# Optimization experiments

Measured on AMD Instinct MI355X. Metric: run time of the kernel, lower is better.

The kernel has to match this reference:

```python
import jax, jax.numpy as jnp
import numpy as np

N_NODES = 50000
N_EDGES = 800000
IN_DIM, HID, OUT_DIM = 32, 96, 1
NEG_SLOPE = 0.2


def _glorot(key, shape):
    fan_in, fan_out = shape[0], shape[-1]
    lim = float(np.sqrt(6.0 / (fan_in + fan_out)))
    return jax.random.uniform(key, shape, jnp.float32, -lim, lim)


def setup_inputs() -> dict:
    key = jax.random.key(0)
    ks = jax.random.split(key, 20)
    inp = {
        "x": jax.random.normal(ks[0], (N_NODES, IN_DIM), jnp.float32),
        "edge_index": jax.random.randint(ks[1], (2, N_EDGES), 0, N_NODES, jnp.int64),
        "edge_weight": jax.random.uniform(ks[2], (N_EDGES,), jnp.float32),
    }
    dims = [(IN_DIM, HID), (HID, HID), (HID, HID), (HID, OUT_DIM)]
    names = ["0", "1", "2", "f"]
    k = 3
    for nm, (di, do) in zip(names, dims):
        inp["W" + nm] = _glorot(ks[k], (di, do)); k += 1
        inp["as" + nm] = _glorot(ks[k], (1, do))[0]; k += 1
        inp["ad" + nm] = _glorot(ks[k], (1, do))[0]; k += 1
        inp["b" + nm] = jnp.zeros((do,), jnp.float32)
    return inp


def _gat_conv(x, src, dst, n, W, a_s, a_d, b):
    # h: [N, out]; per-node attention logits, gathered per edge
    h = x @ W
    es = h @ a_s  # [N]
    ed = h @ a_d  # [N]
    e = jax.nn.leaky_relu(es[src] + ed[dst], NEG_SLOPE)  # [E]
    m = jax.ops.segment_max(e, dst, num_segments=n)  # segment-softmax (stable)
    ex = jnp.exp(e - m[dst])
    s = jax.ops.segment_sum(ex, dst, num_segments=n)
    alpha = ex / s[dst]  # every node has a self loop -> s > 0
    out = jax.ops.segment_sum(alpha[:, None] * h[src], dst, num_segments=n)
    return out + b


def reference(x, edge_index, edge_weight, W0, as0, ad0, b0, W1, as1, ad1, b1,
              W2, as2, ad2, b2, Wf, asf, adf, bf):
    # edge_weight is ignored: PyG GATConv with edge_dim=None drops edge_attr.
    n = x.shape[0]
    loops = jnp.arange(n, dtype=edge_index.dtype)
    src = jnp.concatenate([edge_index[0], loops])  # add_self_loops=True
    dst = jnp.concatenate([edge_index[1], loops])

    # dropout is identity in eval mode
    for (W, a_s, a_d, b) in [(W0, as0, ad0, b0), (W1, as1, ad1, b1), (W2, as2, ad2, b2)]:
        residual = x
        x = _gat_conv(x, src, dst, n, W, a_s, a_d, b)
        if x.shape == residual.shape:
            x = x + residual
        x = jax.nn.relu(x)
    return _gat_conv(x, src, dst, n, Wf, asf, adf, bf)
```

## Files before the change

kernel.cpp:

```cpp
#include <hip/hip_runtime.h>
#include <hip/hip_fp16.h>
#include <math.h>

#define N_NODES 50000
#define N_EDGES 800000
#define E_TOT   (N_EDGES + N_NODES)
#define IN_DIM  32
#define HID     96
#define NEG_SLOPE 0.2f
#define BUCKET  48
#define G_PAD   50
#define NBINS   196
#define BCAP    5120
#define GC_STRIDE 64
#define FILL_EPT 16
#define FILL_NB ((N_EDGES + 256 * FILL_EPT - 1) / (256 * FILL_EPT))
#define AGG_BLOCKS (N_NODES / 16)
#define PREP_BLOCKS ((N_NODES * 32) / 256)
#define WT_BLOCKS (((HID * HID) + 255) / 256)

typedef _Float16 half8v __attribute__((ext_vector_type(8)));
typedef float    float4v __attribute__((ext_vector_type(4)));

static inline int cdiv(long long a, int b) { return (int)((a + b - 1) / b); }

__device__ __forceinline__ int clamp_src(int s) {
    return (int)min((unsigned)s, (unsigned)(N_NODES - 1));
}

__global__ __launch_bounds__(256) void build_prep_kernel(
    const int* __restrict__ ei, unsigned* __restrict__ gcnt,
    unsigned* __restrict__ ebuf,
    const float* __restrict__ x, const float* __restrict__ W0,
    const float* __restrict__ as0, const float* __restrict__ ad0,
    __half* __restrict__ xh, float* __restrict__ es, float* __restrict__ ed,
    const float* __restrict__ W1, const float* __restrict__ W2,
    __half* __restrict__ WT1, __half* __restrict__ WT2) {
    int b = blockIdx.x;
    if (b < FILL_NB) {
        __shared__ unsigned lcnt[256];
        __shared__ unsigned lbase[256];
        int tid = threadIdx.x;
        lcnt[tid] = 0u;
        __syncthreads();
        int e0 = (b * 256 + tid) * FILL_EPT;
        bool val = e0 < N_EDGES;
        unsigned pk[FILL_EPT];
        unsigned short rank[FILL_EPT];
        if (val) {
            #pragma unroll
            for (int q = 0; q < FILL_EPT / 4; ++q) {
                int4 d4 = *(const int4*)(ei + N_EDGES + e0 + q * 4);
                int4 s4 = *(const int4*)(ei + e0 + q * 4);
                int dd[4] = {d4.x, d4.y, d4.z, d4.w};
                int ss[4] = {s4.x, s4.y, s4.z, s4.w};
                #pragma unroll
                for (int k = 0; k < 4; ++k) {
                    int d = clamp_src(dd[k]);
                    int bin = d >> 8;
                    pk[q * 4 + k] = (unsigned)clamp_src(ss[k]) | ((unsigned)(d & 255) << 16)
                                  | ((unsigned)bin << 24);
                    rank[q * 4 + k] = (unsigned short)atomicAdd(&lcnt[bin], 1u);
                }
            }
        }
        __syncthreads();
        if (tid < NBINS) {
            unsigned c = lcnt[tid];
            lbase[tid] = c ? atomicAdd(gcnt + (size_t)tid * GC_STRIDE, c) : 0u;
        }
        __syncthreads();
        if (val) {
            #pragma unroll
            for (int k = 0; k < FILL_EPT; ++k) {
                unsigned bin = pk[k] >> 24;
                unsigned pos = lbase[bin] + rank[k];
                if (pos < BCAP) ebuf[(size_t)bin * BCAP + pos] = pk[k];
            }
        }
        return;
    }
    b -= FILL_NB;
    if (b >= PREP_BLOCKS) {
        int i = (b - PREP_BLOCKS) * 256 + threadIdx.x;
        if (i < HID * HID) {
            int n = i / HID, k = i - n * HID;
            WT1[i] = __float2half(W1[k * HID + n]);
            WT2[i] = __float2half(W2[k * HID + n]);
        }
        return;
    }
    __shared__ float s_us[32], s_ud[32];
    if (threadIdx.x < 64) {
        int k = threadIdx.x & 31;
        int sel = threadIdx.x >> 5;
        const float* a = sel ? ad0 : as0;
        float acc = 0.f;
        #pragma unroll 8
        for (int c = 0; c < HID; ++c) acc += W0[k * HID + c] * a[c];
        if (sel) s_ud[k] = acc; else s_us[k] = acc;
    }
    __syncthreads();
    int idx = b * 256 + threadIdx.x;
    int node = idx >> 5;
    int k = threadIdx.x & 31;
    float xv = x[(size_t)node * 32 + k];
    float xnb = __shfl_xor(xv, 1);
    if ((k & 1) == 0) {
        __half2 h2v = __floats2half2_rn(xv, xnb);
        ((__half2*)xh)[((size_t)node * 32 + k) >> 1] = h2v;
    }
    float ps = xv * s_us[k], pd = xv * s_ud[k];
    #pragma unroll
    for (int o = 16; o; o >>= 1) {
        ps += __shfl_xor(ps, o);
        pd += __shfl_xor(pd, o);
    }
    if (k == 0) { es[node] = ps; ed[node] = pd; }
}

__global__ __launch_bounds__(256) void bucket_build_kernel(
    const unsigned* __restrict__ gcnt, const unsigned* __restrict__ ebuf,
    unsigned* __restrict__ cnt, unsigned short* __restrict__ srcs) {
    __shared__ unsigned short lsr[256][BUCKET];
    __shared__ unsigned lct[256];
    int bin = blockIdx.x, tid = threadIdx.x;
    int nb = bin * 256 + tid;
    lct[tid] = 1u;
    lsr[tid][0] = (unsigned short)min(nb, N_NODES - 1);
    __syncthreads();
    unsigned ec = min(gcnt[(size_t)bin * GC_STRIDE], (unsigned)BCAP);
    for (unsigned j = tid; j < ec; j += 256) {
        unsigned pkv = ebuf[(size_t)bin * BCAP + j];
        unsigned dloc = (pkv >> 16) & 255u;
        unsigned pos = atomicAdd(&lct[dloc], 1u);
        if (pos < BUCKET) lsr[dloc][pos] = (unsigned short)(pkv & 0xFFFFu);
    }
    __syncthreads();
    if (nb < N_NODES) cnt[nb] = min(lct[tid], (unsigned)BUCKET);
    const uint4* ls4 = (const uint4*)&lsr[0][0];
    uint4* gs4 = (uint4*)(srcs + (size_t)bin * 256 * BUCKET);
    for (int i = tid; i < 256 * (BUCKET / 8); i += 256) {
        int node = i / (BUCKET / 8);
        if (bin * 256 + node < N_NODES) gs4[i] = ls4[i];
    }
}

__global__ __launch_bounds__(256) void aggregate32_kernel(
    const unsigned* __restrict__ cnt, const unsigned short* __restrict__ srcs,
    const float* __restrict__ es, const float* __restrict__ ed,
    const __half* __restrict__ xh,
    const float* __restrict__ W0, const float* __restrict__ b0,
    __half* __restrict__ x16a) {
    __shared__ uint2 sh[4][4][G_PAD];
    __shared__ float s_ag[16][33];
    __shared__ float4 s_w0[32][24];
    const float4* W4g = (const float4*)W0;
    for (int i = threadIdx.x; i < 32 * 24; i += 256)
        s_w0[i / 24][i % 24] = W4g[i];

    int lane = threadIdx.x & 63;
    int wv = threadIdx.x >> 6;
    int g = lane >> 4, lin = lane & 15;
    int node = blockIdx.x * 16 + wv * 4 + g;
    size_t row = (size_t)node * BUCKET;
    int deg = min((int)cnt[node], BUCKET);
    float edv = ed[node];

    float lsum = 0.f;
    float4 acc = {0.f, 0.f, 0.f, 0.f};
    const uint2* x2 = (const uint2*)xh;
    int h8sel = lin >> 3;
    int c = lin & 7;

    for (int j = lin; j < deg; j += 16) {
        int s = clamp_src(srcs[row + j]);
        float v = es[s] + edv;
        v = v > 0.f ? v : NEG_SLOPE * v;
        float e = __expf(v);
        uint2 p; p.x = (unsigned)s; p.y = __float_as_uint(e);
        sh[wv][g][j] = p;
        lsum += e;
    }
    int j = 0;
    for (; j + 8 <= deg; j += 8) {
        uint2 p0 = sh[wv][g][j + h8sel];
        uint2 p1 = sh[wv][g][j + 2 + h8sel];
        uint2 p2 = sh[wv][g][j + 4 + h8sel];
        uint2 p3 = sh[wv][g][j + 6 + h8sel];
        uint2 q0 = x2[(size_t)p0.x * 8 + c];
        uint2 q1 = x2[(size_t)p1.x * 8 + c];
        uint2 q2 = x2[(size_t)p2.x * 8 + c];
        uint2 q3 = x2[(size_t)p3.x * 8 + c];
        float e0 = __uint_as_float(p0.y), e1 = __uint_as_float(p1.y);
        float e2 = __uint_as_float(p2.y), e3 = __uint_as_float(p3.y);
        float2 f00 = __half22float2(*(__half2*)&q0.x), f01 = __half22float2(*(__half2*)&q0.y);
        float2 f10 = __half22float2(*(__half2*)&q1.x), f11 = __half22float2(*(__half2*)&q1.y);
        float2 f20 = __half22float2(*(__half2*)&q2.x), f21 = __half22float2(*(__half2*)&q2.y);
        float2 f30 = __half22float2(*(__half2*)&q3.x), f31 = __half22float2(*(__half2*)&q3.y);
        acc.x += e0 * f00.x + e1 * f10.x + e2 * f20.x + e3 * f30.x;
        acc.y += e0 * f00.y + e1 * f10.y + e2 * f20.y + e3 * f30.y;
        acc.z += e0 * f01.x + e1 * f11.x + e2 * f21.x + e3 * f31.x;
        acc.w += e0 * f01.y + e1 * f11.y + e2 * f21.y + e3 * f31.y;
    }
    for (; j + 4 <= deg; j += 4) {
        uint2 p0 = sh[wv][g][j + h8sel];
        uint2 p1 = sh[wv][g][j + 2 + h8sel];
        uint2 q0 = x2[(size_t)p0.x * 8 + c];
        uint2 q1 = x2[(size_t)p1.x * 8 + c];
        float e0 = __uint_as_float(p0.y), e1 = __uint_as_float(p1.y);
        float2 f00 = __half22float2(*(__half2*)&q0.x), f01 = __half22float2(*(__half2*)&q0.y);
        float2 f10 = __half22float2(*(__half2*)&q1.x), f11 = __half22float2(*(__half2*)&q1.y);
        acc.x += e0 * f00.x + e1 * f10.x; acc.y += e0 * f00.y + e1 * f10.y;
        acc.z += e0 * f01.x + e1 * f11.x; acc.w += e0 * f01.y + e1 * f11.y;
    }
    for (; j < deg; j += 2) {
        int idx = j + h8sel;
        if (idx < deg) {
            uint2 p = sh[wv][g][idx];
            uint2 q = x2[(size_t)p.x * 8 + c];
            float e = __uint_as_float(p.y);
            float2 f0 = __half22float2(*(__half2*)&q.x);
            float2 f1 = __half22float2(*(__half2*)&q.y);
            acc.x += e * f0.x; acc.y += e * f0.y;
            acc.z += e * f1.x; acc.w += e * f1.y;
        }
    }
    #pragma unroll
    for (int o = 1; o < 16; o <<= 1) lsum += __shfl_xor(lsum, o);
    acc.x += __shfl_xor(acc.x, 8);
    acc.y += __shfl_xor(acc.y, 8);
    acc.z += __shfl_xor(acc.z, 8);
    acc.w += __shfl_xor(acc.w, 8);
    if (lin < 8) {
        float inv = 1.f / lsum;
        int n = wv * 4 + g;
        s_ag[n][lin * 4 + 0] = acc.x * inv;
        s_ag[n][lin * 4 + 1] = acc.y * inv;
        s_ag[n][lin * 4 + 2] = acc.z * inv;
        s_ag[n][lin * 4 + 3] = acc.w * inv;
    }
    __syncthreads();
    int t = threadIdx.x;
    if (t < 192) {
        int n = t / 12, c8 = t - n * 12;
        int onode = blockIdx.x * 16 + n;
        float4 a0v = {0.f, 0.f, 0.f, 0.f}, a1v = {0.f, 0.f, 0.f, 0.f};
        #pragma unroll 8
        for (int k = 0; k < 32; ++k) {
            float a = s_ag[n][k];
            float4 w0 = s_w0[k][c8 * 2], w1 = s_w0[k][c8 * 2 + 1];
            a0v.x += a * w0.x; a0v.y += a * w0.y; a0v.z += a * w0.z; a0v.w += a * w0.w;
            a1v.x += a * w1.x; a1v.y += a * w1.y; a1v.z += a * w1.z; a1v.w += a * w1.w;
        }
        float4 bb0 = ((const float4*)b0)[c8 * 2], bb1 = ((const float4*)b0)[c8 * 2 + 1];
        float v0 = fmaxf(a0v.x + bb0.x, 0.f), v1 = fmaxf(a0v.y + bb0.y, 0.f);
        float v2 = fmaxf(a0v.z + bb0.z, 0.f), v3 = fmaxf(a0v.w + bb0.w, 0.f);
        float v4 = fmaxf(a1v.x + bb1.x, 0.f), v5 = fmaxf(a1v.y + bb1.y, 0.f);
        float v6 = fmaxf(a1v.z + bb1.z, 0.f), v7 = fmaxf(a1v.w + bb1.w, 0.f);
        __half2 q0 = __floats2half2_rn(v0, v1), q1 = __floats2half2_rn(v2, v3);
        __half2 q2 = __floats2half2_rn(v4, v5), q3 = __floats2half2_rn(v6, v7);
        uint4 st; st.x = *(unsigned*)&q0; st.y = *(unsigned*)&q1;
        st.z = *(unsigned*)&q2; st.w = *(unsigned*)&q3;
        ((uint4*)x16a)[(size_t)onode * 12 + c8] = st;
    }
}

__global__ __launch_bounds__(256) void mfma_gemm96_kernel(
    const __half* __restrict__ x16, const __half* __restrict__ wt,
    const float* __restrict__ a_s, const float* __restrict__ a_d,
    __half* __restrict__ h, float* __restrict__ es, float* __restrict__ ed) {
    __shared__ __align__(16) __half s_t[4][16][104];
    int wid = (int)((blockIdx.x * 256 + threadIdx.x) >> 6);
    if (wid >= N_NODES / 16) return;
    int lane = threadIdx.x & 63;
    int wvl = threadIdx.x >> 6;
    int col = lane & 15, quad = lane >> 4;
    int m0 = wid * 16;
    const __half* arow = x16 + (size_t)(m0 + col) * 96 + quad * 8;
    const __half* brow = wt + (size_t)col * 96 + quad * 8;

    float4v acc[6];
    #pragma unroll
    for (int t = 0; t < 6; ++t) acc[t] = (float4v){0.f, 0.f, 0.f, 0.f};

    #pragma unroll
    for (int ks = 0; ks < 3; ++ks) {
        half8v afrag = *(const half8v*)(arow + ks * 32);
        #pragma unroll
        for (int t = 0; t < 6; ++t) {
            half8v bfrag = *(const half8v*)(brow + (size_t)t * 16 * 96 + ks * 32);
            acc[t] = __builtin_amdgcn_mfma_f32_16x16x32_f16(afrag, bfrag, acc[t], 0, 0, 0);
        }
    }

    float ps0 = 0.f, ps1 = 0.f, ps2 = 0.f, ps3 = 0.f;
    float pd0 = 0.f, pd1 = 0.f, pd2 = 0.f, pd3 = 0.f;
    #pragma unroll
    for (int t = 0; t < 6; ++t) {
        int ch = t * 16 + col;
        float sa = a_s[ch], sd = a_d[ch];
        float v0 = acc[t][0], v1 = acc[t][1], v2 = acc[t][2], v3 = acc[t][3];
        int r0 = quad * 4;
        s_t[wvl][r0 + 0][ch] = __float2half(v0);
        s_t[wvl][r0 + 1][ch] = __float2half(v1);
        s_t[wvl][r0 + 2][ch] = __float2half(v2);
        s_t[wvl][r0 + 3][ch] = __float2half(v3);
        ps0 += v0 * sa; ps1 += v1 * sa; ps2 += v2 * sa; ps3 += v3 * sa;
        pd0 += v0 * sd; pd1 += v1 * sd; pd2 += v2 * sd; pd3 += v3 * sd;
    }
    #pragma unroll
    for (int o = 1; o < 16; o <<= 1) {
        ps0 += __shfl_xor(ps0, o); ps1 += __shfl_xor(ps1, o);
        ps2 += __shfl_xor(ps2, o); ps3 += __shfl_xor(ps3, o);
        pd0 += __shfl_xor(pd0, o); pd1 += __shfl_xor(pd1, o);
        pd2 += __shfl_xor(pd2, o); pd3 += __shfl_xor(pd3, o);
    }
    if (col == 0) {
        int nb = m0 + quad * 4;
        es[nb] = ps0; es[nb + 1] = ps1; es[nb + 2] = ps2; es[nb + 3] = ps3;
        ed[nb] = pd0; ed[nb + 1] = pd1; ed[nb + 2] = pd2; ed[nb + 3] = pd3;
    }
    {
        int trow = lane >> 2, q = lane & 3;
        const uint4* sr = (const uint4*)&s_t[wvl][trow][0];
        uint4* H8 = (uint4*)h;
        size_t rb = (size_t)(m0 + trow) * 12;
        H8[rb + q]     = sr[q];
        H8[rb + q + 4] = sr[q + 4];
        H8[rb + q + 8] = sr[q + 8];
    }
}

__global__ __launch_bounds__(256) void aggregate96_kernel(
    const unsigned* __restrict__ cnt, const unsigned short* __restrict__ srcs,
    const float* __restrict__ es, const float* __restrict__ ed,
    const __half* __restrict__ h, const float* __restrict__ b,
    const __half* __restrict__ res16, __half* __restrict__ out16,
    const float* __restrict__ Wf, float* __restrict__ hfin, int do_relu) {
    __shared__ uint2 sh[4][4][G_PAD];
    int lane = threadIdx.x & 63;
    int wv = threadIdx.x >> 6;
    int g = lane >> 4, lin = lane & 15;
    int node = blockIdx.x * 16 + wv * 4 + g;
    size_t row = (size_t)node * BUCKET;
    int deg = min((int)cnt[node], BUCKET);
    float edv = ed[node];

    float lsum = 0.f;
    float a0 = 0.f, a1 = 0.f, a2 = 0.f, a3 = 0.f, a4 = 0.f, a5 = 0.f, a6 = 0.f, a7 = 0.f;
    const uint4* h8 = (const uint4*)h;
    bool act = (lin < 12);

    for (int j = lin; j < deg; j += 16) {
        int s = clamp_src(srcs[row + j]);
        float v = es[s] + edv;
        v = v > 0.f ? v : NEG_SLOPE * v;
        float e = __expf(v);
        uint2 p; p.x = (unsigned)s; p.y = __float_as_uint(e);
        sh[wv][g][j] = p;
        lsum += e;
    }
    int j = 0;
    for (; j + 4 <= deg; j += 4) {
        uint2 p0 = sh[wv][g][j];
        uint2 p1 = sh[wv][g][j + 1];
        uint2 p2 = sh[wv][g][j + 2];
        uint2 p3 = sh[wv][g][j + 3];
        if (act) {
            uint4 q0 = h8[(size_t)p0.x * 12 + lin];
            uint4 q1 = h8[(size_t)p1.x * 12 + lin];
            uint4 q2 = h8[(size_t)p2.x * 12 + lin];
            uint4 q3 = h8[(size_t)p3.x * 12 + lin];
            float e0 = __uint_as_float(p0.y), e1 = __uint_as_float(p1.y);
            float e2 = __uint_as_float(p2.y), e3 = __uint_as_float(p3.y);
            float2 fa0 = __half22float2(*(__half2*)&q0.x), fa1 = __half22float2(*(__half2*)&q0.y);
            float2 fa2 = __half22float2(*(__half2*)&q0.z), fa3 = __half22float2(*(__half2*)&q0.w);
            float2 fb0 = __half22float2(*(__half2*)&q1.x), fb1 = __half22float2(*(__half2*)&q1.y);
            float2 fb2 = __half22float2(*(__half2*)&q1.z), fb3 = __half22float2(*(__half2*)&q1.w);
            float2 fc0 = __half22float2(*(__half2*)&q2.x), fc1 = __half22float2(*(__half2*)&q2.y);
            float2 fc2 = __half22float2(*(__half2*)&q2.z), fc3 = __half22float2(*(__half2*)&q2.w);
            float2 fd0 = __half22float2(*(__half2*)&q3.x), fd1 = __half22float2(*(__half2*)&q3.y);
            float2 fd2 = __half22float2(*(__half2*)&q3.z), fd3 = __half22float2(*(__half2*)&q3.w);
            a0 += e0 * fa0.x + e1 * fb0.x + e2 * fc0.x + e3 * fd0.x;
            a1 += e0 * fa0.y + e1 * fb0.y + e2 * fc0.y + e3 * fd0.y;
            a2 += e0 * fa1.x + e1 * fb1.x + e2 * fc1.x + e3 * fd1.x;
            a3 += e0 * fa1.y + e1 * fb1.y + e2 * fc1.y + e3 * fd1.y;
            a4 += e0 * fa2.x + e1 * fb2.x + e2 * fc2.x + e3 * fd2.x;
            a5 += e0 * fa2.y + e1 * fb2.y + e2 * fc2.y + e3 * fd2.y;
            a6 += e0 * fa3.x + e1 * fb3.x + e2 * fc3.x + e3 * fd3.x;
            a7 += e0 * fa3.y + e1 * fb3.y + e2 * fc3.y + e3 * fd3.y;
        }
    }
    for (; j < deg; ++j) {
        uint2 p = sh[wv][g][j];
        if (act) {
            uint4 q = h8[(size_t)p.x * 12 + lin];
            float e = __uint_as_float(p.y);
            float2 f0 = __half22float2(*(__half2*)&q.x);
            float2 f1 = __half22float2(*(__half2*)&q.y);
            float2 f2 = __half22float2(*(__half2*)&q.z);
            float2 f3 = __half22float2(*(__half2*)&q.w);
            a0 += e * f0.x; a1 += e * f0.y;
            a2 += e * f1.x; a3 += e * f1.y;
            a4 += e * f2.x; a5 += e * f2.y;
            a6 += e * f3.x; a7 += e * f3.y;
        }
    }
    #pragma unroll
    for (int o = 1; o < 16; o <<= 1) lsum += __shfl_xor(lsum, o);

    float pfin = 0.f;
    if (act) {
        float inv = 1.f / lsum;
        const float4* b4 = (const float4*)b;
        float4 bb0 = b4[lin * 2], bb1 = b4[lin * 2 + 1];
        float v0 = a0 * inv + bb0.x, v1 = a1 * inv + bb0.y;
        float v2 = a2 * inv + bb0.z, v3 = a3 * inv + bb0.w;
        float v4 = a4 * inv + bb1.x, v5 = a5 * inv + bb1.y;
        float v6 = a6 * inv + bb1.z, v7 = a7 * inv + bb1.w;
        if (res16) {
            uint4 rr = ((const uint4*)res16)[(size_t)node * 12 + lin];
            float2 r0 = __half22float2(*(__half2*)&rr.x);
            float2 r1 = __half22float2(*(__half2*)&rr.y);
            float2 r2 = __half22float2(*(__half2*)&rr.z);
            float2 r3 = __half22float2(*(__half2*)&rr.w);
            v0 += r0.x; v1 += r0.y; v2 += r1.x; v3 += r1.y;
            v4 += r2.x; v5 += r2.y; v6 += r3.x; v7 += r3.y;
        }
        if (do_relu) {
            v0 = fmaxf(v0, 0.f); v1 = fmaxf(v1, 0.f); v2 = fmaxf(v2, 0.f); v3 = fmaxf(v3, 0.f);
            v4 = fmaxf(v4, 0.f); v5 = fmaxf(v5, 0.f); v6 = fmaxf(v6, 0.f); v7 = fmaxf(v7, 0.f);
        }
        if (out16) {
            __half2 q0 = __floats2half2_rn(v0, v1), q1 = __floats2half2_rn(v2, v3);
            __half2 q2 = __floats2half2_rn(v4, v5), q3 = __floats2half2_rn(v6, v7);
            uint4 st; st.x = *(unsigned*)&q0; st.y = *(unsigned*)&q1;
            st.z = *(unsigned*)&q2; st.w = *(unsigned*)&q3;
            ((uint4*)out16)[(size_t)node * 12 + lin] = st;
        }
        if (hfin) {
            const float4* w4 = (const float4*)Wf;
            float4 wf0 = w4[lin * 2], wf1 = w4[lin * 2 + 1];
            pfin = v0 * wf0.x + v1 * wf0.y + v2 * wf0.z + v3 * wf0.w
                 + v4 * wf1.x + v5 * wf1.y + v6 * wf1.z + v7 * wf1.w;
        }
    }
    if (hfin) {
        #pragma unroll
        for (int o = 1; o < 16; o <<= 1) pfin += __shfl_xor(pfin, o);
        if (lin == 0) hfin[node] = pfin;
    }
}

__global__ __launch_bounds__(256) void aggregate1_kernel(
    const unsigned* __restrict__ cnt, const unsigned short* __restrict__ srcs,
    const float* __restrict__ hfin, const float* __restrict__ asf,
    const float* __restrict__ adf, const float* __restrict__ bf,
    float* __restrict__ out) {
    int lane = threadIdx.x & 63;
    int wv = threadIdx.x >> 6;
    int g = lane >> 4, lin = lane & 15;
    int node = blockIdx.x * 16 + wv * 4 + g;
    size_t row = (size_t)node * BUCKET;
    int deg = min((int)cnt[node], BUCKET);
    float as0 = asf[0], ad0 = adf[0];
    float edv = hfin[node] * ad0;

    float lsum = 0.f, acc = 0.f;
    for (int j = lin; j < deg; j += 16) {
        int s = clamp_src(srcs[row + j]);
        float hs = hfin[s];
        float v = as0 * hs + edv;
        v = v > 0.f ? v : NEG_SLOPE * v;
        float ex = __expf(v);
        lsum += ex;
        acc += ex * hs;
    }
    #pragma unroll
    for (int o = 1; o < 16; o <<= 1) {
        lsum += __shfl_xor(lsum, o);
        acc  += __shfl_xor(acc, o);
    }
    if (lin == 0) out[node] = acc / lsum + bf[0];
}


extern "C" void kernel_launch(void* const* d_in, const int* in_sizes, int n_in,
                              void* d_out, int out_size, void* d_ws, size_t ws_size,
                              hipStream_t stream) {
    const float* x  = (const float*)d_in[0];
    const int*   ei = (const int*)d_in[1];
    const float* W0 = (const float*)d_in[3];
    const float* as0 = (const float*)d_in[4];
    const float* ad0 = (const float*)d_in[5];
    const float* b0 = (const float*)d_in[6];
    const float* W1 = (const float*)d_in[7];
    const float* as1 = (const float*)d_in[8];
    const float* ad1 = (const float*)d_in[9];
    const float* b1 = (const float*)d_in[10];
    const float* W2 = (const float*)d_in[11];
    const float* as2 = (const float*)d_in[12];
    const float* ad2 = (const float*)d_in[13];
    const float* b2 = (const float*)d_in[14];
    const float* Wf = (const float*)d_in[15];
    const float* asf = (const float*)d_in[16];
    const float* adf = (const float*)d_in[17];
    const float* bf = (const float*)d_in[18];

    float* out = (float*)d_out;

    float* Hf = (float*)d_ws;
    __half* H16 = (__half*)Hf;
    float* ES = Hf + (long long)N_NODES * HID;
    float* ED = ES + N_NODES;
    unsigned* CNT = (unsigned*)(ED + N_NODES);
    unsigned short* SRCS = (unsigned short*)(CNT + N_NODES);
    __half* X16A = (__half*)(SRCS + (size_t)N_NODES * BUCKET);
    __half* X16B = X16A + (size_t)N_NODES * HID;
    __half* WT1 = X16B + (size_t)N_NODES * HID;
    __half* WT2 = WT1 + HID * HID;
    float* HFIN = (float*)(WT2 + HID * HID);
    __half* XH = (__half*)(HFIN + N_NODES);
    unsigned* GCNT = (unsigned*)(XH + (size_t)N_NODES * 32);
    unsigned* EBUF = GCNT + (size_t)NBINS * GC_STRIDE;

    hipMemsetAsync(GCNT, 0, (size_t)NBINS * GC_STRIDE * sizeof(unsigned), stream);
    build_prep_kernel<<<FILL_NB + PREP_BLOCKS + WT_BLOCKS, 256, 0, stream>>>(
        ei, GCNT, EBUF, x, W0, as0, ad0, XH, ES, ED, W1, W2, WT1, WT2);
    bucket_build_kernel<<<NBINS, 256, 0, stream>>>(GCNT, EBUF, CNT, SRCS);

    const int mfma_blocks = cdiv(N_NODES / 16, 4);

    aggregate32_kernel<<<AGG_BLOCKS, 256, 0, stream>>>(CNT, SRCS, ES, ED, XH, W0, b0, X16A);

    mfma_gemm96_kernel<<<mfma_blocks, 256, 0, stream>>>(X16A, WT1, as1, ad1, H16, ES, ED);
    aggregate96_kernel<<<AGG_BLOCKS, 256, 0, stream>>>(
        CNT, SRCS, ES, ED, H16, b1, X16A, X16B, nullptr, nullptr, 1);

    mfma_gemm96_kernel<<<mfma_blocks, 256, 0, stream>>>(X16B, WT2, as2, ad2, H16, ES, ED);
    aggregate96_kernel<<<AGG_BLOCKS, 256, 0, stream>>>(
        CNT, SRCS, ES, ED, H16, b2, X16B, nullptr, Wf, HFIN, 1);

    aggregate1_kernel<<<AGG_BLOCKS, 256, 0, stream>>>(CNT, SRCS, HFIN, asf, adf, bf, out);
}
```

Before: 239.2 us.

## Fuse 96-wide MFMA projection into preceding aggregation kernels

Removes the standalone mfma_gemm96 kernel launches by having each aggregation block stage its 16 output rows in shared memory and run the next layer's MFMA projection plus attention-logit reduction in one wave. Double-buffers H and ES/ED so a kernel can write the next layer's projections while others still read the current ones. This saves two launches and a global reread of the hidden features, at the cost of extra shared memory and a serialized single-wave epilogue per block that leaves three waves idle.

```diff
diff --git a/kernel.cpp b/kernel.cpp
--- a/kernel.cpp
+++ b/kernel.cpp
@@ -26,6 +26,65 @@
 
 __device__ __forceinline__ int clamp_src(int s) {
     return (int)min((unsigned)s, (unsigned)(N_NODES - 1));
+}
+
+__device__ __forceinline__ void mfma_tile_epilogue(
+    const __half* s_x , __half* s_t ,
+    const __half* __restrict__ wt, const float* __restrict__ a_s,
+    const float* __restrict__ a_d, __half* __restrict__ h,
+    float* __restrict__ es, float* __restrict__ ed, int m0, int lane) {
+    int col = lane & 15, quad = lane >> 4;
+    const __half* arow = s_x + col * 104 + quad * 8;
+    const __half* brow = wt + (size_t)col * 96 + quad * 8;
+
+    float4v acc[6];
+    #pragma unroll
+    for (int t = 0; t < 6; ++t) acc[t] = (float4v){0.f, 0.f, 0.f, 0.f};
+    #pragma unroll
+    for (int ks = 0; ks < 3; ++ks) {
+        half8v afrag = *(const half8v*)(arow + ks * 32);
+        #pragma unroll
+        for (int t = 0; t < 6; ++t) {
+            half8v bfrag = *(const half8v*)(brow + (size_t)t * 16 * 96 + ks * 32);
+            acc[t] = __builtin_amdgcn_mfma_f32_16x16x32_f16(afrag, bfrag, acc[t], 0, 0, 0);
+        }
+    }
+    float ps0 = 0.f, ps1 = 0.f, ps2 = 0.f, ps3 = 0.f;
+    float pd0 = 0.f, pd1 = 0.f, pd2 = 0.f, pd3 = 0.f;
+    #pragma unroll
+    for (int t = 0; t < 6; ++t) {
+        int ch = t * 16 + col;
+        float sa = a_s[ch], sd = a_d[ch];
+        float v0 = acc[t][0], v1 = acc[t][1], v2 = acc[t][2], v3 = acc[t][3];
+        int r0 = quad * 4;
+        s_t[(r0 + 0) * 104 + ch] = __float2half(v0);
+        s_t[(r0 + 1) * 104 + ch] = __float2half(v1);
+        s_t[(r0 + 2) * 104 + ch] = __float2half(v2);
+        s_t[(r0 + 3) * 104 + ch] = __float2half(v3);
+        ps0 += v0 * sa; ps1 += v1 * sa; ps2 += v2 * sa; ps3 += v3 * sa;
+        pd0 += v0 * sd; pd1 += v1 * sd; pd2 += v2 * sd; pd3 += v3 * sd;
+    }
+    #pragma unroll
+    for (int o = 1; o < 16; o <<= 1) {
+        ps0 += __shfl_xor(ps0, o); ps1 += __shfl_xor(ps1, o);
+        ps2 += __shfl_xor(ps2, o); ps3 += __shfl_xor(ps3, o);
+        pd0 += __shfl_xor(pd0, o); pd1 += __shfl_xor(pd1, o);
+        pd2 += __shfl_xor(pd2, o); pd3 += __shfl_xor(pd3, o);
+    }
+    if (col == 0) {
+        int nb = m0 + quad * 4;
+        es[nb] = ps0; es[nb + 1] = ps1; es[nb + 2] = ps2; es[nb + 3] = ps3;
+        ed[nb] = pd0; ed[nb + 1] = pd1; ed[nb + 2] = pd2; ed[nb + 3] = pd3;
+    }
+    {
+        int trow = lane >> 2, q = lane & 3;
+        const uint4* sr = (const uint4*)(s_t + trow * 104);
+        uint4* H8 = (uint4*)h;
+        size_t rb = (size_t)(m0 + trow) * 12;
+        H8[rb + q]     = sr[q];
+        H8[rb + q + 4] = sr[q + 4];
+        H8[rb + q + 8] = sr[q + 8];
+    }
 }
 
 __global__ __launch_bounds__(256) void build_prep_kernel(
@@ -151,10 +210,15 @@
     const float* __restrict__ es, const float* __restrict__ ed,
     const __half* __restrict__ xh,
     const float* __restrict__ W0, const float* __restrict__ b0,
-    __half* __restrict__ x16a) {
+    __half* __restrict__ x16a,
+    const __half* __restrict__ wt1, const float* __restrict__ as1,
+    const float* __restrict__ ad1, __half* __restrict__ hA,
+    float* __restrict__ es2, float* __restrict__ ed2) {
     __shared__ uint2 sh[4][4][G_PAD];
     __shared__ float s_ag[16][33];
     __shared__ float4 s_w0[32][24];
+    __shared__ __align__(16) __half s_x[16 * 104];
+    __shared__ __align__(16) __half s_t[16 * 104];
     const float4* W4g = (const float4*)W0;
     for (int i = threadIdx.x; i < 32 * 24; i += 256)
         s_w0[i / 24][i % 24] = W4g[i];
@@ -263,73 +327,12 @@
         uint4 st; st.x = *(unsigned*)&q0; st.y = *(unsigned*)&q1;
         st.z = *(unsigned*)&q2; st.w = *(unsigned*)&q3;
         ((uint4*)x16a)[(size_t)onode * 12 + c8] = st;
-    }
-}
-
-__global__ __launch_bounds__(256) void mfma_gemm96_kernel(
-    const __half* __restrict__ x16, const __half* __restrict__ wt,
-    const float* __restrict__ a_s, const float* __restrict__ a_d,
-    __half* __restrict__ h, float* __restrict__ es, float* __restrict__ ed) {
-    __shared__ __align__(16) __half s_t[4][16][104];
-    int wid = (int)((blockIdx.x * 256 + threadIdx.x) >> 6);
-    if (wid >= N_NODES / 16) return;
-    int lane = threadIdx.x & 63;
-    int wvl = threadIdx.x >> 6;
-    int col = lane & 15, quad = lane >> 4;
-    int m0 = wid * 16;
-    const __half* arow = x16 + (size_t)(m0 + col) * 96 + quad * 8;
-    const __half* brow = wt + (size_t)col * 96 + quad * 8;
-
-    float4v acc[6];
-    #pragma unroll
-    for (int t = 0; t < 6; ++t) acc[t] = (float4v){0.f, 0.f, 0.f, 0.f};
-
-    #pragma unroll
-    for (int ks = 0; ks < 3; ++ks) {
-        half8v afrag = *(const half8v*)(arow + ks * 32);
-        #pragma unroll
-        for (int t = 0; t < 6; ++t) {
-            half8v bfrag = *(const half8v*)(brow + (size_t)t * 16 * 96 + ks * 32);
-            acc[t] = __builtin_amdgcn_mfma_f32_16x16x32_f16(afrag, bfrag, acc[t], 0, 0, 0);
-        }
-    }
-
-    float ps0 = 0.f, ps1 = 0.f, ps2 = 0.f, ps3 = 0.f;
-    float pd0 = 0.f, pd1 = 0.f, pd2 = 0.f, pd3 = 0.f;
-    #pragma unroll
-    for (int t = 0; t < 6; ++t) {
-        int ch = t * 16 + col;
-        float sa = a_s[ch], sd = a_d[ch];
-        float v0 = acc[t][0], v1 = acc[t][1], v2 = acc[t][2], v3 = acc[t][3];
-        int r0 = quad * 4;
-        s_t[wvl][r0 + 0][ch] = __float2half(v0);
-        s_t[wvl][r0 + 1][ch] = __float2half(v1);
-        s_t[wvl][r0 + 2][ch] = __float2half(v2);
-        s_t[wvl][r0 + 3][ch] = __float2half(v3);
-        ps0 += v0 * sa; ps1 += v1 * sa; ps2 += v2 * sa; ps3 += v3 * sa;
-        pd0 += v0 * sd; pd1 += v1 * sd; pd2 += v2 * sd; pd3 += v3 * sd;
-    }
-    #pragma unroll
-    for (int o = 1; o < 16; o <<= 1) {
-        ps0 += __shfl_xor(ps0, o); ps1 += __shfl_xor(ps1, o);
-        ps2 += __shfl_xor(ps2, o); ps3 += __shfl_xor(ps3, o);
-        pd0 += __shfl_xor(pd0, o); pd1 += __shfl_xor(pd1, o);
-        pd2 += __shfl_xor(pd2, o); pd3 += __shfl_xor(pd3, o);
-    }
-    if (col == 0) {
-        int nb = m0 + quad * 4;
-        es[nb] = ps0; es[nb + 1] = ps1; es[nb + 2] = ps2; es[nb + 3] = ps3;
-        ed[nb] = pd0; ed[nb + 1] = pd1; ed[nb + 2] = pd2; ed[nb + 3] = pd3;
-    }
-    {
-        int trow = lane >> 2, q = lane & 3;
-        const uint4* sr = (const uint4*)&s_t[wvl][trow][0];
-        uint4* H8 = (uint4*)h;
-        size_t rb = (size_t)(m0 + trow) * 12;
-        H8[rb + q]     = sr[q];
-        H8[rb + q + 4] = sr[q + 4];
-        H8[rb + q + 8] = sr[q + 8];
-    }
+        *(uint4*)(s_x + n * 104 + c8 * 8) = st;
+    }
+    __syncthreads();
+    if (threadIdx.x < 64)
+        mfma_tile_epilogue(s_x, s_t, wt1, as1, ad1, hA, es2, ed2,
+                           blockIdx.x * 16, lane);
 }
 
 __global__ __launch_bounds__(256) void aggregate96_kernel(
@@ -337,8 +340,13 @@
     const float* __restrict__ es, const float* __restrict__ ed,
     const __half* __restrict__ h, const float* __restrict__ b,
     const __half* __restrict__ res16, __half* __restrict__ out16,
-    const float* __restrict__ Wf, float* __restrict__ hfin, int do_relu) {
+    const float* __restrict__ Wf, float* __restrict__ hfin,
+    const __half* __restrict__ wtproj, const float* __restrict__ as_n,
+    const float* __restrict__ ad_n, __half* __restrict__ h_out,
+    float* __restrict__ es_n, float* __restrict__ ed_n) {
     __shared__ uint2 sh[4][4][G_PAD];
+    __shared__ __align__(16) __half s_x[16 * 104];
+    __shared__ __align__(16) __half s_t[16 * 104];
     int lane = threadIdx.x & 63;
     int wv = threadIdx.x >> 6;
     int g = lane >> 4, lin = lane & 15;
@@ -428,16 +436,16 @@
             v0 += r0.x; v1 += r0.y; v2 += r1.x; v3 += r1.y;
             v4 += r2.x; v5 += r2.y; v6 += r3.x; v7 += r3.y;
         }
-        if (do_relu) {
-            v0 = fmaxf(v0, 0.f); v1 = fmaxf(v1, 0.f); v2 = fmaxf(v2, 0.f); v3 = fmaxf(v3, 0.f);
-            v4 = fmaxf(v4, 0.f); v5 = fmaxf(v5, 0.f); v6 = fmaxf(v6, 0.f); v7 = fmaxf(v7, 0.f);
-        }
-        if (out16) {
-            __half2 q0 = __floats2half2_rn(v0, v1), q1 = __floats2half2_rn(v2, v3);
-            __half2 q2 = __floats2half2_rn(v4, v5), q3 = __floats2half2_rn(v6, v7);
-            uint4 st; st.x = *(unsigned*)&q0; st.y = *(unsigned*)&q1;
-            st.z = *(unsigned*)&q2; st.w = *(unsigned*)&q3;
-            ((uint4*)out16)[(size_t)node * 12 + lin] = st;
+        v0 = fmaxf(v0, 0.f); v1 = fmaxf(v1, 0.f); v2 = fmaxf(v2, 0.f); v3 = fmaxf(v3, 0.f);
+        v4 = fmaxf(v4, 0.f); v5 = fmaxf(v5, 0.f); v6 = fmaxf(v6, 0.f); v7 = fmaxf(v7, 0.f);
+        __half2 q0 = __floats2half2_rn(v0, v1), q1 = __floats2half2_rn(v2, v3);
+        __half2 q2 = __floats2half2_rn(v4, v5), q3 = __floats2half2_rn(v6, v7);
+        uint4 st; st.x = *(unsigned*)&q0; st.y = *(unsigned*)&q1;
+        st.z = *(unsigned*)&q2; st.w = *(unsigned*)&q3;
+        if (out16) ((uint4*)out16)[(size_t)node * 12 + lin] = st;
+        if (wtproj) {
+            int n = wv * 4 + g;
+            *(uint4*)(s_x + n * 104 + lin * 8) = st;
         }
         if (hfin) {
             const float4* w4 = (const float4*)Wf;
@@ -450,6 +458,12 @@
         #pragma unroll
         for (int o = 1; o < 16; o <<= 1) pfin += __shfl_xor(pfin, o);
         if (lin == 0) hfin[node] = pfin;
+    }
+    if (wtproj) {
+        __syncthreads();
+        if (threadIdx.x < 64)
+            mfma_tile_epilogue(s_x, s_t, wtproj, as_n, ad_n, h_out, es_n, ed_n,
+                               blockIdx.x * 16, lane);
     }
 }
 
@@ -511,7 +525,8 @@
     float* out = (float*)d_out;
 
     float* Hf = (float*)d_ws;
-    __half* H16 = (__half*)Hf;
+    __half* H16A = (__half*)Hf;
+    __half* H16B = H16A + (size_t)N_NODES * HID;
     float* ES = Hf + (long long)N_NODES * HID;
     float* ED = ES + N_NODES;
     unsigned* CNT = (unsigned*)(ED + N_NODES);
@@ -524,23 +539,24 @@
     __half* XH = (__half*)(HFIN + N_NODES);
     unsigned* GCNT = (unsigned*)(XH + (size_t)N_NODES * 32);
     unsigned* EBUF = GCNT + (size_t)NBINS * GC_STRIDE;
+    float* ES2 = (float*)(EBUF + (size_t)NBINS * BCAP);
+    float* ED2 = ES2 + N_NODES;
 
     hipMemsetAsync(GCNT, 0, (size_t)NBINS * GC_STRIDE * sizeof(unsigned), stream);
     build_prep_kernel<<<FILL_NB + PREP_BLOCKS + WT_BLOCKS, 256, 0, stream>>>(
         ei, GCNT, EBUF, x, W0, as0, ad0, XH, ES, ED, W1, W2, WT1, WT2);
     bucket_build_kernel<<<NBINS, 256, 0, stream>>>(GCNT, EBUF, CNT, SRCS);
 
-    const int mfma_blocks = cdiv(N_NODES / 16, 4);
-
-    aggregate32_kernel<<<AGG_BLOCKS, 256, 0, stream>>>(CNT, SRCS, ES, ED, XH, W0, b0, X16A);
-
-    mfma_gemm96_kernel<<<mfma_blocks, 256, 0, stream>>>(X16A, WT1, as1, ad1, H16, ES, ED);
+    aggregate32_kernel<<<AGG_BLOCKS, 256, 0, stream>>>(
+        CNT, SRCS, ES, ED, XH, W0, b0, X16A, WT1, as1, ad1, H16A, ES2, ED2);
+
     aggregate96_kernel<<<AGG_BLOCKS, 256, 0, stream>>>(
-        CNT, SRCS, ES, ED, H16, b1, X16A, X16B, nullptr, nullptr, 1);
-
-    mfma_gemm96_kernel<<<mfma_blocks, 256, 0, stream>>>(X16B, WT2, as2, ad2, H16, ES, ED);
+        CNT, SRCS, ES2, ED2, H16A, b1, X16A, X16B, nullptr, nullptr,
+        WT2, as2, ad2, H16B, ES, ED);
+
     aggregate96_kernel<<<AGG_BLOCKS, 256, 0, stream>>>(
-        CNT, SRCS, ES, ED, H16, b2, X16B, nullptr, Wf, HFIN, 1);
+        CNT, SRCS, ES, ED, H16B, b2, X16B, nullptr, Wf, HFIN,
+        nullptr, nullptr, nullptr, nullptr, nullptr, nullptr);
 
     aggregate1_kernel<<<AGG_BLOCKS, 256, 0, stream>>>(CNT, SRCS, HFIN, asf, adf, bf, out);
 }
```

Result: no change. 234.9 us (-1.8%).
